# Kernel optimization log

Hardware: AMD Instinct MI355X
Metric: run time of the kernel (lower is better)

## Reference

```python
import jax, jax.numpy as jnp
import numpy as np

I_SZ, H_SZ, M_SZ, D_SZ, T_LEN = 256, 512, 16384, 256, 128


def setup_inputs() -> dict:
    key = jax.random.key(0)
    ks = iter(jax.random.split(key, 48))

    def rn(shape, s=0.05):
        return jax.random.normal(next(ks), shape, dtype=jnp.float32) * s

    Hd, D = H_SZ, D_SZ
    inp = {
        "inputs": rn((T_LEN, 1, I_SZ), 1.0),
        "memory0": rn((M_SZ, D), 0.01),            # register_buffer: randn*0.01
        "read_w0": jnp.zeros((M_SZ,), jnp.float32),
        "write_w0": jnp.zeros((M_SZ,), jnp.float32),
        "W_ih": rn((4 * Hd, I_SZ + D)),             # LSTM input->gates (i,f,g,o)
        "W_hh": rn((4 * Hd, Hd)),
        "b_ih": jnp.zeros((4 * Hd,), jnp.float32),
        "b_hh": jnp.zeros((4 * Hd,), jnp.float32),
        "Wo": rn((I_SZ, Hd + D)),                   # output_layer
        "bo": jnp.zeros((I_SZ,), jnp.float32),
    }
    for p in ("r", "w"):  # read head / write head addressing params
        inp[p + "_Wk"] = rn((D, Hd)); inp[p + "_bk"] = jnp.zeros((D,), jnp.float32)
        inp[p + "_Wb"] = rn((1, Hd)); inp[p + "_bb"] = jnp.zeros((1,), jnp.float32)
        inp[p + "_Wg"] = rn((1, Hd)); inp[p + "_bg"] = jnp.zeros((1,), jnp.float32)
        inp[p + "_Ws"] = rn((3, Hd)); inp[p + "_bs"] = jnp.zeros((3,), jnp.float32)
        inp[p + "_Wp"] = rn((1, Hd)); inp[p + "_bp"] = jnp.zeros((1,), jnp.float32)
    inp["w_We"] = rn((D, Hd)); inp["w_be"] = jnp.zeros((D,), jnp.float32)  # erase
    inp["w_Wa"] = rn((D, Hd)); inp["w_ba"] = jnp.zeros((D,), jnp.float32)  # add
    return inp


def _attend(co, mem, prev_w, Wk, bk, Wb, bb, Wg, bg, Ws, bs, Wp, bp):
    # co: (1,H), mem: (M,D), prev_w: (M,) -> (M,)
    key = co @ Wk.T + bk                                   # (1,D)
    beta = jax.nn.softplus(co @ Wb.T + bb)                 # (1,1) key strength
    kn = key / jnp.maximum(jnp.linalg.norm(key, axis=-1, keepdims=True), 1e-12)
    mn = mem / jnp.maximum(jnp.linalg.norm(mem, axis=-1, keepdims=True), 1e-12)
    cw = jax.nn.softmax(beta * (kn @ mn.T), axis=-1)       # (1,M) content weights
    g = jax.nn.sigmoid(co @ Wg.T + bg)                     # interpolation gate
    gw = g * cw + (1.0 - g) * prev_w[None, :]
    s = jax.nn.softmax(co @ Ws.T + bs, axis=-1)            # (1,3) shift kernel
    shifted = (s[:, 0:1] * jnp.roll(gw, -1, axis=-1)
               + s[:, 1:2] * gw
               + s[:, 2:3] * jnp.roll(gw, 1, axis=-1))
    gamma = jax.nn.softplus(co @ Wp.T + bp) + 1.0          # sharpening >= 1
    w = shifted ** gamma
    return (w / (w.sum(-1, keepdims=True) + 1e-8))[0]


def reference(inputs, memory0, read_w0, write_w0, W_ih, W_hh, b_ih, b_hh, Wo, bo,
              r_Wk, r_bk, r_Wb, r_bb, r_Wg, r_bg, r_Ws, r_bs, r_Wp, r_bp,
              w_Wk, w_bk, w_Wb, w_bb, w_Wg, w_bg, w_Ws, w_bs, w_Wp, w_bp,
              w_We, w_be, w_Wa, w_ba):
    H = W_hh.shape[1]

    def step(carry, x_t):
        mem, rw, ww, h, c = carry
        read_vec = rw @ mem                                  # (D,) read old memory
        ci = jnp.concatenate([x_t[0], read_vec])[None, :]    # (1, I+D)
        gates = ci @ W_ih.T + b_ih + h @ W_hh.T + b_hh       # (1, 4H)
        i_, f_, g_, o_ = jnp.split(gates, 4, axis=-1)
        c_new = jax.nn.sigmoid(f_) * c + jax.nn.sigmoid(i_) * jnp.tanh(g_)
        h_new = jax.nn.sigmoid(o_) * jnp.tanh(c_new)
        co = h_new                                           # controller output (1,H)
        ww_new = _attend(co, mem, ww, w_Wk, w_bk, w_Wb, w_bb, w_Wg, w_bg, w_Ws, w_bs, w_Wp, w_bp)
        erase = jax.nn.sigmoid(co @ w_We.T + w_be)[0]        # (D,)
        add = (co @ w_Wa.T + w_ba)[0]                        # (D,)
        mem_new = mem * (1.0 - ww_new[:, None] * erase[None, :]) + ww_new[:, None] * add[None, :]
        rw_new = _attend(co, mem_new, rw, r_Wk, r_bk, r_Wb, r_bb, r_Wg, r_bg, r_Ws, r_bs, r_Wp, r_bp)
        out = jnp.concatenate([co[0], read_vec])[None, :] @ Wo.T + bo  # (1, I)
        return (mem_new, rw_new, ww_new, h_new, c_new), out

    init = (memory0, read_w0, write_w0,
            jnp.zeros((1, H), inputs.dtype), jnp.zeros((1, H), inputs.dtype))
    _, outs = jax.lax.scan(step, init, inputs)               # (T,1,I)
    return outs
```

## Files before the change

### kernel.cpp

```cpp
#include <hip/hip_runtime.h>
#include <math.h>


#define NBLK 128
#define NTHR 512
#define Msz  16384
#define Dsz  256
#define Hsz  512
#define Isz  256
#define Tlen 128
#define RPB  128
#define NG   16

#define FXS  1073741824.0f
#define FXSI (1.0 / 1073741824.0)
#define CNT1 (1ull << 48)

struct Params { const float* in[34]; float* out; float* ws; };

__device__ __forceinline__ float wred64(float v){
#pragma unroll
  for (int o = 32; o > 0; o >>= 1) v += __shfl_xor(v, o, 64);
  return v;
}
__device__ __forceinline__ float wred32(float v){
#pragma unroll
  for (int o = 16; o > 0; o >>= 1) v += __shfl_xor(v, o, 32);
  return v;
}
__device__ __forceinline__ float qsum4(float v){
  v += __uint_as_float(__builtin_amdgcn_mov_dpp(__float_as_uint(v), 0xB1, 0xF, 0xF, true));
  v += __uint_as_float(__builtin_amdgcn_mov_dpp(__float_as_uint(v), 0x4E, 0xF, 0xF, true));
  return v;
}
__device__ __forceinline__ float sigm(float x){ return 1.f / (1.f + __expf(-x)); }
__device__ __forceinline__ float softplusf(float x){ return (x > 20.f) ? x : log1pf(__expf(x)); }

__device__ __forceinline__ void gstore(float* p, float v){
  __hip_atomic_store(p, v, __ATOMIC_RELAXED, __HIP_MEMORY_SCOPE_AGENT);
}
__device__ __forceinline__ float gload(const float* p){
  return __hip_atomic_load(p, __ATOMIC_RELAXED, __HIP_MEMORY_SCOPE_AGENT);
}
__device__ __forceinline__ void gstore64(unsigned long long* p, unsigned long long v){
  __hip_atomic_store(p, v, __ATOMIC_RELAXED, __HIP_MEMORY_SCOPE_AGENT);
}
__device__ __forceinline__ unsigned long long gload64(const unsigned long long* p){
  return __hip_atomic_load(p, __ATOMIC_RELAXED, __HIP_MEMORY_SCOPE_AGENT);
}
__device__ __forceinline__ void lbar(){
  __builtin_amdgcn_s_waitcnt(0xC07F);
  __builtin_amdgcn_s_barrier();
}
__device__ __forceinline__ float pollw(const unsigned long long* p, unsigned want){
  unsigned long long k;
  do { k = gload64(p); } while ((int)((unsigned)(k >> 32) - want) < 0);
  return __uint_as_float((unsigned)k);
}
__device__ __forceinline__ unsigned long long fxpack(float v){
  return CNT1 + (unsigned long long)(v * FXS);
}

__global__ void __launch_bounds__(NTHR, 1)
ntm_kernel(Params P)
{
  const int b   = blockIdx.x;
  const int tid = threadIdx.x;
  const int wv  = tid >> 6;
  const int ln  = tid & 63;

  const float* inputs  = P.in[0];
  const float* mem0    = P.in[1];
  const float* read_w0 = P.in[2];
  const float* write_w0= P.in[3];
  const float* W_ih = P.in[4];
  const float* W_hh = P.in[5];
  const float* b_ih = P.in[6];
  const float* b_hh = P.in[7];
  const float* Wo   = P.in[8];
  const float* bo   = P.in[9];
  const float* r_Wk = P.in[10]; const float* r_bk = P.in[11];
  const float* r_Wb = P.in[12]; const float* r_bb = P.in[13];
  const float* r_Wg = P.in[14]; const float* r_bg = P.in[15];
  const float* r_Ws = P.in[16]; const float* r_bs = P.in[17];
  const float* r_Wp = P.in[18]; const float* r_bp = P.in[19];
  const float* w_Wk = P.in[20]; const float* w_bk = P.in[21];
  const float* w_Wb = P.in[22]; const float* w_bb = P.in[23];
  const float* w_Wg = P.in[24]; const float* w_bg = P.in[25];
  const float* w_Ws = P.in[26]; const float* w_bs = P.in[27];
  const float* w_Wp = P.in[28]; const float* w_bp = P.in[29];
  const float* w_We = P.in[30]; const float* w_be = P.in[31];
  const float* w_Wa = P.in[32]; const float* w_ba = P.in[33];
  float* out = P.out;

  float* ws = P.ws;
  float* PA = ws;
  float* PB = ws + 4096;
  unsigned long long* U    = (unsigned long long*)(ws + 8192);
  unsigned long long* hpub = U;
  unsigned long long* ppub = U + 1024;
  unsigned long long* wEF  = U + 2320;
  unsigned long long* wPF  = wEF + 128;
  unsigned long long* wEL  = wPF + 128;
  unsigned long long* wPL  = wEL + 128;
  unsigned long long* rEF  = wPL + 128;
  unsigned long long* rPF  = rEF + 128;
  unsigned long long* rEL  = rPF + 128;
  unsigned long long* rPL  = rEL + 128;
  unsigned long long* redD = rPL + 128;
  unsigned long long* redF = redD + Tlen;
  unsigned long long* redH = redF + Tlen;
  unsigned long long* redJ = redH + Tlen;
  unsigned long long* redI = redJ + Tlen;
  float* Pbuf[2] = { PA, PB };

  __shared__ float s_mem[RPB * Dsz];
  __shared__ float s_co[Hsz];
  __shared__ float s_a[256], s_b[256], s_c[256];
  __shared__ float s_rv[256];
  __shared__ float s_norm[RPB];
  __shared__ float s_e[RPB];
  __shared__ float s_bw[RPB];
  __shared__ float s_rw[RPB];
  __shared__ float s_ww[RPB];
  __shared__ float s_A1[RPB], s_A2[RPB], s_B1[RPB], s_B0[RPB];
  __shared__ float s_dot[RPB];
  __shared__ float s_red[8];
  __shared__ float s_lg[16];
  __shared__ float s_scal[16];
  __shared__ float s_w2[2];
  __shared__ float s_cst[4];
  __shared__ float s_bd[4];
  __shared__ float s_pub;
  __shared__ float s_gval;

  auto redWait = [&](unsigned long long* slot)->float{
    if (tid == 0){
      unsigned long long k;
      do { k = gload64(slot); } while ((unsigned)(k >> 48) < (unsigned)NBLK);
      s_gval = (float)((double)(k & 0xFFFFFFFFFFFFull) * FXSI);
    }
    lbar();
    return s_gval;
  };

  auto bred512 = [&](float v)->float{
    v = wred64(v);
    lbar();
    if (ln == 0) s_red[wv] = v;
    lbar();
    return s_red[0] + s_red[1] + s_red[2] + s_red[3]
         + s_red[4] + s_red[5] + s_red[6] + s_red[7];
  };

  auto shiftSharpen = [&](int si, float* s_prevw, float S, unsigned long long* slot){
    float g     = sigm(s_scal[si + 1]);
    float gamma = softplusf(s_scal[si + 2]) + 1.f;
    float a0 = s_scal[si + 3], a1 = s_scal[si + 4], a2 = s_scal[si + 5];
    float mx = fmaxf(a0, fmaxf(a1, a2));
    float e0 = __expf(a0 - mx), e1 = __expf(a1 - mx), e2 = __expf(a2 - mx);
    float idn = 1.f / (e0 + e1 + e2);
    float s0 = e0 * idn, s1 = e1 * idn, s2 = e2 * idn;
    float invS = 1.f / S;
    float w = 0.f;
    if (tid < RPB){
      float gc = g * invS, gp = 1.f - g;
      float em = s_e[tid],  pm = s_prevw[tid];
      float e1n = (tid < RPB-1) ? s_e[tid+1]     : s_bd[0];
      float p1n = (tid < RPB-1) ? s_prevw[tid+1] : s_bd[1];
      float e2n = (tid > 0)     ? s_e[tid-1]     : s_bd[2];
      float p2n = (tid > 0)     ? s_prevw[tid-1] : s_bd[3];
      float gwm = gc * em  + gp * pm;
      float gw1 = gc * e1n + gp * p1n;
      float gw2 = gc * e2n + gp * p2n;
      float sh = s0 * gw1 + s1 * gwm + s2 * gw2;
      w = powf(sh, gamma);
      s_bw[tid] = w;
    }
    float tot = wred64(w);
    if (ln == 0 && wv < 2) s_w2[wv] = tot;
    lbar();
    if (tid == 0){
      float T2 = s_w2[0] + s_w2[1];
      s_pub = T2;
      if (slot) atomicAdd(slot, fxpack(T2));
    }
  };

  auto gemvXH = [&]()->float{
    int dd = tid >> 5, l = tid & 31;
    int r = (dd >> 2) * Hsz + (b << 2) + (dd & 3);
    const float* wi = W_ih + (size_t)r * (Isz + Dsz);
    const float* wh = W_hh + (size_t)r * Hsz;
    float acc = 0.f;
#pragma unroll
    for (int it = 0; it < 2; ++it){
      int k = it * 128 + l * 4;
      float4 a = *(const float4*)(wi + k);
      float4 x = *(const float4*)(&s_a[k]);
      acc += a.x*x.x + a.y*x.y + a.z*x.z + a.w*x.w;
    }
#pragma unroll
    for (int it = 0; it < 4; ++it){
      int k = it * 128 + l * 4;
      float4 hw = *(const float4*)(wh + k);
      float4 hv = *(const float4*)(&s_co[k]);
      acc += hw.x*hv.x + hw.y*hv.y + hw.z*hv.z + hw.w*hv.w;
    }
    return acc;
  };

  float Srcarry = 1.f;
  float accxh   = 0.f;

  {
    if (b < NG && tid < 256){ gstore(&PA[b*256 + tid], 0.f); gstore(&PB[b*256 + tid], 0.f); }
    if (tid < RPB){
      s_rw[tid] = read_w0[b * RPB + tid];
      s_ww[tid] = write_w0[b * RPB + tid];
    }
    if (tid < 4) s_cst[tid] = 0.f;
    s_co[tid] = 0.f;
    __syncthreads();
    if (tid == 0) atomicAdd(redI + 0, CNT1);
    redWait(redI + 0);
  }

  {
#pragma unroll 1
    for (int it = 0; it < 16; ++it){
      int ml = it * 8 + wv;
      int m  = b * RPB + ml;
      float4 v = *(const float4*)(mem0 + (size_t)m * Dsz + ln * 4);
      *(float4*)(&s_mem[ml * Dsz + ln * 4]) = v;
      float n2 = wred64(v.x*v.x + v.y*v.y + v.z*v.z + v.w*v.w);
      if (ln == 0) s_norm[ml] = sqrtf(n2);
    }
    lbar();
    int col = tid & 255, half = tid >> 8;
    float acc = 0.f;
#pragma unroll 1
    for (int j = half * 64; j < half * 64 + 64; ++j) acc += s_rw[j] * s_mem[j * Dsz + col];
    if (half == 0) s_a[col] = acc;
    lbar();
    if (half == 1) atomicAdd(&PB[(b & (NG-1)) * 256 + col], acc + s_a[col]);
    __syncthreads();
    if (tid < 256) s_a[tid] = inputs[tid];
    if (tid == 0) atomicAdd(redI + 1, CNT1);
    lbar();
    accxh = gemvXH();
    redWait(redI + 1);
  }

  for (int t = 0; t < Tlen; ++t){
    const unsigned TT = (unsigned)(t + 3);
    const unsigned long long tg = (unsigned long long)TT << 32;
    float* Pcur = Pbuf[t & 1];
    float* Prd  = Pbuf[(t + 1) & 1];

    {
      float SrDiv = (t == 0) ? 1.f : (Srcarry + 1e-8f);
      if (t > 0 && tid < RPB) s_rw[tid] = s_bw[tid] / SrDiv;
      if (tid < 256){
        float rvv = 0.f;
#pragma unroll
        for (int p = 0; p < NG; ++p) rvv += gload(&Prd[p * 256 + tid]);
        s_rv[tid] = rvv / SrDiv;
      }
      lbar();
      int dd = tid >> 5, l = tid & 31;
      int r = (dd >> 2) * Hsz + (b << 2) + (dd & 3);
      const float* wi = W_ih + (size_t)r * (Isz + Dsz) + Isz;
      float acc = accxh;
#pragma unroll
      for (int it = 0; it < 2; ++it){
        int k = it * 128 + l * 4;
        float4 a = *(const float4*)(wi + k);
        float4 x = *(const float4*)(&s_rv[k]);
        acc += a.x*x.x + a.y*x.y + a.z*x.z + a.w*x.w;
      }
      acc = wred32(acc);
      if (l == 0) s_lg[dd] = acc + b_ih[r] + b_hh[r];
      lbar();
      if (tid < 4){
        float iv = s_lg[tid], fv = s_lg[4 + tid], gv = s_lg[8 + tid], ov = s_lg[12 + tid];
        float cn = sigm(fv) * s_cst[tid] + sigm(iv) * tanhf(gv);
        s_cst[tid] = cn;
        float hn = sigm(ov) * tanhf(cn);
        gstore64(&hpub[(size_t)b * 8 + tid], tg | (unsigned long long)__float_as_uint(hn));
      }
    }

    {
      s_co[tid] = pollw(&hpub[(size_t)(tid >> 2) * 8 + (tid & 3)], TT);
      lbar();
#pragma unroll
      for (int qi = 0; qi < 2; ++qi){
        int q = qi * 8 + wv;
        int slot = q * 128 + b;
        if (slot < 1292){
          const float* Wrow = nullptr; float bias = 0.f; int len = 512;
          int mode = 0;
          if (slot < 256){ Wrow = w_Wk + (size_t)slot * Hsz; bias = w_bk[slot]; }
          else if (slot < 512){ int i = slot - 256; Wrow = w_We + (size_t)i * Hsz; bias = w_be[i]; mode = 1; }
          else if (slot < 768){ int i = slot - 512; Wrow = w_Wa + (size_t)i * Hsz; bias = w_ba[i]; }
          else if (slot < 1024){ int i = slot - 768; Wrow = r_Wk + (size_t)i * Hsz; bias = r_bk[i]; }
          else if (slot < 1280){ int i = slot - 1024; Wrow = Wo + (size_t)i * (Hsz + Dsz); bias = bo[i]; len = 768; mode = 2; }
          else {
            int i = slot - 1280;
            int ii = (i >= 6) ? i - 6 : i;
            bool rh = (i >= 6);
            const float *Wt, *bt; int row = 0;
            if (ii == 0){ Wt = rh ? r_Wb : w_Wb; bt = rh ? r_bb : w_bb; }
            else if (ii == 1){ Wt = rh ? r_Wg : w_Wg; bt = rh ? r_bg : w_bg; }
            else if (ii == 2){ Wt = rh ? r_Wp : w_Wp; bt = rh ? r_bp : w_bp; }
            else { Wt = rh ? r_Ws : w_Ws; bt = rh ? r_bs : w_bs; row = ii - 3; }
            Wrow = Wt + (size_t)row * Hsz; bias = bt[row];
          }
          float acc = 0.f;
          if (len == 512){
            int k = ln * 8;
            float4 a0 = *(const float4*)(Wrow + k);
            float4 a1 = *(const float4*)(Wrow + k + 4);
            float4 c0 = *(const float4*)(&s_co[k]);
            float4 c1 = *(const float4*)(&s_co[k + 4]);
            acc = a0.x*c0.x + a0.y*c0.y + a0.z*c0.z + a0.w*c0.w
                + a1.x*c1.x + a1.y*c1.y + a1.z*c1.z + a1.w*c1.w;
          } else {
            int k = ln * 4;
            float4 w0 = *(const float4*)(Wrow + k);
            float4 w1 = *(const float4*)(Wrow + 256 + k);
            float4 w2 = *(const float4*)(Wrow + 512 + k);
            float4 c0 = *(const float4*)(&s_co[k]);
            float4 c1 = *(const float4*)(&s_co[256 + k]);
            float4 r0 = *(const float4*)(&s_rv[k]);
            acc = w0.x*c0.x + w0.y*c0.y + w0.z*c0.z + w0.w*c0.w
                + w1.x*c1.x + w1.y*c1.y + w1.z*c1.z + w1.w*c1.w
                + w2.x*r0.x + w2.y*r0.y + w2.z*r0.z + w2.w*r0.w;
          }
          acc = wred64(acc);
          if (ln == 0){
            float v = acc + bias;
            if (mode == 1) v = sigm(v);
            if (mode == 2) out[(size_t)t * Isz + (slot - 1024)] = v;
            else gstore64(&ppub[slot], tg | (unsigned long long)__float_as_uint(v));
          }
        }
      }
    }

    if (t == Tlen - 1) break;

    float betaR = 0.f, invbkR = 0.f;

    {
      float* Pnx = Pbuf[(t + 1) & 1];
      if (b < NG && tid < 256) gstore(&Pnx[b * 256 + tid], 0.f);
      if (tid < 256) s_a[tid] = pollw(&ppub[tid], TT);
      else if (tid < 268) s_scal[tid - 256] = pollw(&ppub[1280 + (tid - 256)], TT);
      lbar();
      float nk2 = bred512((tid < 256) ? s_a[tid] * s_a[tid] : 0.f);
      float beta  = softplusf(s_scal[0]);
      float invbk = beta / fmaxf(sqrtf(nk2), 1e-12f);
      int row = tid >> 2, q = tid & 3;
      const float* mrow = &s_mem[row * Dsz];
      float d = 0.f;
#pragma unroll
      for (int k = 0; k < 16; ++k){
        int c = (q + 4 * ((k + row) & 15)) * 4;
        float4 mv = *(const float4*)(mrow + c);
        float4 kv = *(const float4*)(&s_a[c]);
        d += mv.x*kv.x + mv.y*kv.y + mv.z*kv.z + mv.w*kv.w;
      }
      d = qsum4(d);
      if (q == 0) s_dot[row] = d;
      lbar();
      float e = 0.f;
      if (tid < RPB){
        float score = s_dot[tid] * invbk / fmaxf(s_norm[tid], 1e-12f);
        e = __expf(score - beta);
        s_e[tid] = e;
      }
      float tot = wred64(e);
      if (ln == 0 && wv < 2) s_w2[wv] = tot;
      lbar();
      if (tid == 0){
        float T = s_w2[0] + s_w2[1];
        gstore64(&wEF[b], tg | (unsigned long long)__float_as_uint(s_e[0]));
        gstore64(&wPF[b], tg | (unsigned long long)__float_as_uint(s_ww[0]));
        gstore64(&wEL[b], tg | (unsigned long long)__float_as_uint(s_e[RPB-1]));
        gstore64(&wPL[b], tg | (unsigned long long)__float_as_uint(s_ww[RPB-1]));
        atomicAdd(redD + t, fxpack(T));
      }
    }

    {
      if (tid < 256) s_a[tid] = pollw(&ppub[256 + tid], TT);
      else           s_b[tid - 256] = pollw(&ppub[512 + (tid - 256)], TT);
      if (tid < 256) s_c[tid] = pollw(&ppub[768 + tid], TT);
      float nk2r = bred512((tid < 256) ? s_c[tid] * s_c[tid] : 0.f);
      betaR  = softplusf(s_scal[6]);
      invbkR = betaR / fmaxf(sqrtf(nk2r), 1e-12f);
      int row = tid >> 2, q = tid & 3;
      const float* mrow = &s_mem[row * Dsz];
      float mq = 0.f, qq = 0.f, qk = 0.f, mk = 0.f;
#pragma unroll
      for (int k = 0; k < 16; ++k){
        int c = (q + 4 * ((k + row) & 15)) * 4;
        float4 mv = *(const float4*)(mrow + c);
        float4 er = *(const float4*)(&s_a[c]);
        float4 ad = *(const float4*)(&s_b[c]);
        float4 kr = *(const float4*)(&s_c[c]);
        float qx = ad.x - mv.x * er.x;
        float qy = ad.y - mv.y * er.y;
        float qz = ad.z - mv.z * er.z;
        float qw = ad.w - mv.w * er.w;
        mq += mv.x*qx + mv.y*qy + mv.z*qz + mv.w*qw;
        qq += qx*qx + qy*qy + qz*qz + qw*qw;
        qk += qx*kr.x + qy*kr.y + qz*kr.z + qw*kr.w;
        mk += mv.x*kr.x + mv.y*kr.y + mv.z*kr.z + mv.w*kr.w;
      }
      mq = qsum4(mq); qq = qsum4(qq); qk = qsum4(qk); mk = qsum4(mk);
      if (q == 0){ s_A1[row] = 2.f*mq; s_A2[row] = qq; s_B1[row] = qk; s_B0[row] = mk; }
    }

    {
      if (wv == 0 && ln < 4){
        const unsigned long long* bp = (ln == 0) ? &wEF[(b + 1) & (NBLK-1)]
                               : (ln == 1) ? &wPF[(b + 1) & (NBLK-1)]
                               : (ln == 2) ? &wEL[(b - 1) & (NBLK-1)]
                                           : &wPL[(b - 1) & (NBLK-1)];
        s_bd[ln] = pollw(bp, TT);
      }
      float S_w = redWait(redD + t);
      shiftSharpen(0, s_ww, S_w, redF + t);
    }

    {
      float Sw = redWait(redF + t);
      float invSw = 1.f / (Sw + 1e-8f);
      float4 er4 = *(const float4*)(&s_a[ln * 4]);
      float4 ad4 = *(const float4*)(&s_b[ln * 4]);
      float e = 0.f;
      if (tid < RPB){
        float wwm = s_bw[tid] * invSw;
        s_ww[tid] = wwm;
        float A0 = s_norm[tid] * s_norm[tid];
        float n2 = fmaf(wwm, fmaf(wwm, s_A2[tid], s_A1[tid]), A0);
        float dt = fmaf(wwm, s_B1[tid], s_B0[tid]);
        float nr = sqrtf(fmaxf(n2, 0.f));
        s_norm[tid] = nr;
        float score = dt * invbkR / fmaxf(nr, 1e-12f);
        e = __expf(score - betaR);
        s_e[tid] = e;
      }
      float tot = wred64(e);
      if (ln == 0 && wv < 2) s_w2[wv] = tot;
      lbar();
      if (tid == 0){
        float T2 = s_w2[0] + s_w2[1];
        gstore64(&rEF[b], tg | (unsigned long long)__float_as_uint(s_e[0]));
        gstore64(&rPF[b], tg | (unsigned long long)__float_as_uint(s_rw[0]));
        gstore64(&rEL[b], tg | (unsigned long long)__float_as_uint(s_e[RPB-1]));
        gstore64(&rPL[b], tg | (unsigned long long)__float_as_uint(s_rw[RPB-1]));
        atomicAdd(redH + t, fxpack(T2));
      }
#pragma unroll 1
      for (int it = 0; it < 16; ++it){
        int ml = it * 8 + wv;
        int off = ml * Dsz + ln * 4;
        float wwm = s_bw[ml] * invSw;
        float4 mv = *(const float4*)(&s_mem[off]);
        float4 nv;
        nv.x = fmaf(wwm, ad4.x - mv.x * er4.x, mv.x);
        nv.y = fmaf(wwm, ad4.y - mv.y * er4.y, mv.y);
        nv.z = fmaf(wwm, ad4.z - mv.z * er4.z, mv.z);
        nv.w = fmaf(wwm, ad4.w - mv.w * er4.w, mv.w);
        *(float4*)(&s_mem[off]) = nv;
      }
    }

    {
      if (wv == 0 && ln < 4){
        const unsigned long long* bp = (ln == 0) ? &rEF[(b + 1) & (NBLK-1)]
                               : (ln == 1) ? &rPF[(b + 1) & (NBLK-1)]
                               : (ln == 2) ? &rEL[(b - 1) & (NBLK-1)]
                                           : &rPL[(b - 1) & (NBLK-1)];
        s_bd[ln] = pollw(bp, TT);
      }
      float S_r = redWait(redH + t);
      shiftSharpen(6, s_rw, S_r, nullptr);
      lbar();
      int col = tid & 255, half = tid >> 8;
      float acc = 0.f;
#pragma unroll 1
      for (int j = half * 64; j < half * 64 + 64; ++j) acc += s_bw[j] * s_mem[j * Dsz + col];
      if (half == 0) s_a[col] = acc;
      lbar();
      if (half == 1) atomicAdd(&Pcur[(b & (NG-1)) * 256 + col], acc + s_a[col]);
      __syncthreads();
      if (tid == 0) atomicAdd(redJ + t, fxpack(s_pub));
      if (tid < 256) s_a[tid] = inputs[(size_t)(t + 1) * Isz + tid];
      lbar();
      accxh = gemvXH();
      Srcarry = redWait(redJ + t);
    }
  }
}

extern "C" void kernel_launch(void* const* d_in, const int* in_sizes, int n_in,
                              void* d_out, int out_size, void* d_ws, size_t ws_size,
                              hipStream_t stream)
{
  (void)in_sizes; (void)out_size;
  if (n_in < 34) return;
  if (ws_size < (size_t)98304) return;
  Params P;
  for (int i = 0; i < 34; ++i) P.in[i] = (const float*)d_in[i];
  P.out = (float*)d_out;
  P.ws  = (float*)d_ws;
  hipLaunchKernelGGL(ntm_kernel, dim3(NBLK), dim3(NTHR), 0, stream, P);
}
```

Before: 3.631 ms.

## Spread grid-wide reduction atomics across eight slots to cut contention

The per-timestep cross-block reductions (redD, redF, redH, redJ) used to send all 128 blocks' atomicAdds to a single 64-bit counter. Each reduction now has eight counters, chosen by block index mod 8, so sixteen blocks share each one. The waiting thread polls all eight and sums their counts and values. The fixed-point scale also moves from 2^30 to 2^32 and is computed in double, giving finer precision but less headroom before the 48-bit value field overflows. Erase, add and read-key vectors get their own shared buffers instead of reusing s_a/s_b/s_c, so s_a can be overwritten without clobbering them.

```diff
diff --git a/kernel.cpp b/kernel.cpp
--- a/kernel.cpp
+++ b/kernel.cpp
@@ -12,8 +12,6 @@
 #define RPB  128
 #define NG   16
 
-#define FXS  1073741824.0f
-#define FXSI (1.0 / 1073741824.0)
 #define CNT1 (1ull << 48)
 
 struct Params { const float* in[34]; float* out; float* ws; };
@@ -58,7 +56,7 @@
   return __uint_as_float((unsigned)k);
 }
 __device__ __forceinline__ unsigned long long fxpack(float v){
-  return CNT1 + (unsigned long long)(v * FXS);
+  return CNT1 + (unsigned long long)((double)v * 4294967296.0);
 }
 
 __global__ void __launch_bounds__(NTHR, 1)
@@ -96,7 +94,7 @@
   float* ws = P.ws;
   float* PA = ws;
   float* PB = ws + 4096;
-  unsigned long long* U    = (unsigned long long*)(ws + 8192);
+  unsigned long long* U = (unsigned long long*)(ws + 8192);
   unsigned long long* hpub = U;
   unsigned long long* ppub = U + 1024;
   unsigned long long* wEF  = U + 2320;
@@ -107,16 +105,18 @@
   unsigned long long* rPF  = rEF + 128;
   unsigned long long* rEL  = rPF + 128;
   unsigned long long* rPL  = rEL + 128;
-  unsigned long long* redD = rPL + 128;
-  unsigned long long* redF = redD + Tlen;
-  unsigned long long* redH = redF + Tlen;
-  unsigned long long* redJ = redH + Tlen;
-  unsigned long long* redI = redJ + Tlen;
+  unsigned long long* redD = U + 3344;
+  unsigned long long* redF = redD + 8 * Tlen;
+  unsigned long long* redH = redF + 8 * Tlen;
+  unsigned long long* redJ = redH + 8 * Tlen;
+  unsigned long long* redI = redJ + 8 * Tlen;
   float* Pbuf[2] = { PA, PB };
+  const int slot = b & 7;
 
   __shared__ float s_mem[RPB * Dsz];
   __shared__ float s_co[Hsz];
-  __shared__ float s_a[256], s_b[256], s_c[256];
+  __shared__ float s_a[256];
+  __shared__ float s_er[256], s_ad[256], s_kr[256];
   __shared__ float s_rv[256];
   __shared__ float s_norm[RPB];
   __shared__ float s_e[RPB];
@@ -134,11 +134,32 @@
   __shared__ float s_pub;
   __shared__ float s_gval;
 
-  auto redWait = [&](unsigned long long* slot)->float{
+  auto redWait8 = [&](unsigned long long* base, int t)->float{
+    if (tid == 0){
+      unsigned long long k0,k1,k2,k3,k4,k5,k6,k7;
+      for (;;){
+        k0 = gload64(base + 0*Tlen + t); k1 = gload64(base + 1*Tlen + t);
+        k2 = gload64(base + 2*Tlen + t); k3 = gload64(base + 3*Tlen + t);
+        k4 = gload64(base + 4*Tlen + t); k5 = gload64(base + 5*Tlen + t);
+        k6 = gload64(base + 6*Tlen + t); k7 = gload64(base + 7*Tlen + t);
+        unsigned c = (unsigned)(k0>>48) + (unsigned)(k1>>48)
+                   + (unsigned)(k2>>48) + (unsigned)(k3>>48)
+                   + (unsigned)(k4>>48) + (unsigned)(k5>>48)
+                   + (unsigned)(k6>>48) + (unsigned)(k7>>48);
+        if (c >= (unsigned)NBLK) break;
+      }
+      const unsigned long long m = 0xFFFFFFFFFFFFull;
+      unsigned long long s = (k0&m)+(k1&m)+(k2&m)+(k3&m)+(k4&m)+(k5&m)+(k6&m)+(k7&m);
+      s_gval = (float)((double)s * (1.0 / 4294967296.0));
+    }
+    lbar();
+    return s_gval;
+  };
+  auto redWait1 = [&](unsigned long long* p)->float{
     if (tid == 0){
       unsigned long long k;
-      do { k = gload64(slot); } while ((unsigned)(k >> 48) < (unsigned)NBLK);
-      s_gval = (float)((double)(k & 0xFFFFFFFFFFFFull) * FXSI);
+      do { k = gload64(p); } while ((unsigned)(k >> 48) < (unsigned)NBLK);
+      s_gval = (float)((double)(k & 0xFFFFFFFFFFFFull) * (1.0 / 4294967296.0));
     }
     lbar();
     return s_gval;
@@ -153,7 +174,7 @@
          + s_red[4] + s_red[5] + s_red[6] + s_red[7];
   };
 
-  auto shiftSharpen = [&](int si, float* s_prevw, float S, unsigned long long* slot){
+  auto shiftSharpen = [&](int si, float* s_prevw, float S, unsigned long long* slotp){
     float g     = sigm(s_scal[si + 1]);
     float gamma = softplusf(s_scal[si + 2]) + 1.f;
     float a0 = s_scal[si + 3], a1 = s_scal[si + 4], a2 = s_scal[si + 5];
@@ -183,7 +204,7 @@
     if (tid == 0){
       float T2 = s_w2[0] + s_w2[1];
       s_pub = T2;
-      if (slot) atomicAdd(slot, fxpack(T2));
+      if (slotp) atomicAdd(slotp, fxpack(T2));
     }
   };
 
@@ -223,7 +244,7 @@
     s_co[tid] = 0.f;
     __syncthreads();
     if (tid == 0) atomicAdd(redI + 0, CNT1);
-    redWait(redI + 0);
+    redWait1(redI + 0);
   }
 
   {
@@ -249,7 +270,7 @@
     if (tid == 0) atomicAdd(redI + 1, CNT1);
     lbar();
     accxh = gemvXH();
-    redWait(redI + 1);
+    redWait1(redI + 1);
   }
 
   for (int t = 0; t < Tlen; ++t){
@@ -297,17 +318,17 @@
 #pragma unroll
       for (int qi = 0; qi < 2; ++qi){
         int q = qi * 8 + wv;
-        int slot = q * 128 + b;
-        if (slot < 1292){
+        int pslot = q * 128 + b;
+        if (pslot < 1292){
           const float* Wrow = nullptr; float bias = 0.f; int len = 512;
           int mode = 0;
-          if (slot < 256){ Wrow = w_Wk + (size_t)slot * Hsz; bias = w_bk[slot]; }
-          else if (slot < 512){ int i = slot - 256; Wrow = w_We + (size_t)i * Hsz; bias = w_be[i]; mode = 1; }
-          else if (slot < 768){ int i = slot - 512; Wrow = w_Wa + (size_t)i * Hsz; bias = w_ba[i]; }
-          else if (slot < 1024){ int i = slot - 768; Wrow = r_Wk + (size_t)i * Hsz; bias = r_bk[i]; }
-          else if (slot < 1280){ int i = slot - 1024; Wrow = Wo + (size_t)i * (Hsz + Dsz); bias = bo[i]; len = 768; mode = 2; }
+          if (pslot < 256){ Wrow = w_Wk + (size_t)pslot * Hsz; bias = w_bk[pslot]; }
+          else if (pslot < 512){ int i = pslot - 256; Wrow = w_We + (size_t)i * Hsz; bias = w_be[i]; mode = 1; }
+          else if (pslot < 768){ int i = pslot - 512; Wrow = w_Wa + (size_t)i * Hsz; bias = w_ba[i]; }
+          else if (pslot < 1024){ int i = pslot - 768; Wrow = r_Wk + (size_t)i * Hsz; bias = r_bk[i]; }
+          else if (pslot < 1280){ int i = pslot - 1024; Wrow = Wo + (size_t)i * (Hsz + Dsz); bias = bo[i]; len = 768; mode = 2; }
           else {
-            int i = slot - 1280;
+            int i = pslot - 1280;
             int ii = (i >= 6) ? i - 6 : i;
             bool rh = (i >= 6);
             const float *Wt, *bt; int row = 0;
@@ -342,8 +363,8 @@
           if (ln == 0){
             float v = acc + bias;
             if (mode == 1) v = sigm(v);
-            if (mode == 2) out[(size_t)t * Isz + (slot - 1024)] = v;
-            else gstore64(&ppub[slot], tg | (unsigned long long)__float_as_uint(v));
+            if (mode == 2) out[(size_t)t * Isz + (pslot - 1024)] = v;
+            else gstore64(&ppub[pslot], tg | (unsigned long long)__float_as_uint(v));
           }
         }
       }
@@ -390,15 +411,15 @@
         gstore64(&wPF[b], tg | (unsigned long long)__float_as_uint(s_ww[0]));
         gstore64(&wEL[b], tg | (unsigned long long)__float_as_uint(s_e[RPB-1]));
         gstore64(&wPL[b], tg | (unsigned long long)__float_as_uint(s_ww[RPB-1]));
-        atomicAdd(redD + t, fxpack(T));
-      }
-    }
-
-    {
-      if (tid < 256) s_a[tid] = pollw(&ppub[256 + tid], TT);
-      else           s_b[tid - 256] = pollw(&ppub[512 + (tid - 256)], TT);
-      if (tid < 256) s_c[tid] = pollw(&ppub[768 + tid], TT);
-      float nk2r = bred512((tid < 256) ? s_c[tid] * s_c[tid] : 0.f);
+        atomicAdd(redD + slot * Tlen + t, fxpack(T));
+      }
+    }
+
+    {
+      if (tid < 256) s_er[tid] = pollw(&ppub[256 + tid], TT);
+      else           s_ad[tid - 256] = pollw(&ppub[512 + (tid - 256)], TT);
+      if (tid < 256) s_kr[tid] = pollw(&ppub[768 + tid], TT);
+      float nk2r = bred512((tid < 256) ? s_kr[tid] * s_kr[tid] : 0.f);
       betaR  = softplusf(s_scal[6]);
       invbkR = betaR / fmaxf(sqrtf(nk2r), 1e-12f);
       int row = tid >> 2, q = tid & 3;
@@ -408,9 +429,9 @@
       for (int k = 0; k < 16; ++k){
         int c = (q + 4 * ((k + row) & 15)) * 4;
         float4 mv = *(const float4*)(mrow + c);
-        float4 er = *(const float4*)(&s_a[c]);
-        float4 ad = *(const float4*)(&s_b[c]);
-        float4 kr = *(const float4*)(&s_c[c]);
+        float4 er = *(const float4*)(&s_er[c]);
+        float4 ad = *(const float4*)(&s_ad[c]);
+        float4 kr = *(const float4*)(&s_kr[c]);
         float qx = ad.x - mv.x * er.x;
         float qy = ad.y - mv.y * er.y;
         float qz = ad.z - mv.z * er.z;
@@ -432,15 +453,15 @@
                                            : &wPL[(b - 1) & (NBLK-1)];
         s_bd[ln] = pollw(bp, TT);
       }
-      float S_w = redWait(redD + t);
-      shiftSharpen(0, s_ww, S_w, redF + t);
-    }
-
-    {
-      float Sw = redWait(redF + t);
+      float S_w = redWait8(redD, t);
+      shiftSharpen(0, s_ww, S_w, redF + slot * Tlen + t);
+    }
+
+    {
+      float Sw = redWait8(redF, t);
       float invSw = 1.f / (Sw + 1e-8f);
-      float4 er4 = *(const float4*)(&s_a[ln * 4]);
-      float4 ad4 = *(const float4*)(&s_b[ln * 4]);
+      float4 er4 = *(const float4*)(&s_er[ln * 4]);
+      float4 ad4 = *(const float4*)(&s_ad[ln * 4]);
       float e = 0.f;
       if (tid < RPB){
         float wwm = s_bw[tid] * invSw;
@@ -463,7 +484,7 @@
         gstore64(&rPF[b], tg | (unsigned long long)__float_as_uint(s_rw[0]));
         gstore64(&rEL[b], tg | (unsigned long long)__float_as_uint(s_e[RPB-1]));
         gstore64(&rPL[b], tg | (unsigned long long)__float_as_uint(s_rw[RPB-1]));
-        atomicAdd(redH + t, fxpack(T2));
+        atomicAdd(redH + slot * Tlen + t, fxpack(T2));
       }
 #pragma unroll 1
       for (int it = 0; it < 16; ++it){
@@ -488,7 +509,7 @@
                                            : &rPL[(b - 1) & (NBLK-1)];
         s_bd[ln] = pollw(bp, TT);
       }
-      float S_r = redWait(redH + t);
+      float S_r = redWait8(redH, t);
       shiftSharpen(6, s_rw, S_r, nullptr);
       lbar();
       int col = tid & 255, half = tid >> 8;
@@ -499,11 +520,11 @@
       lbar();
       if (half == 1) atomicAdd(&Pcur[(b & (NG-1)) * 256 + col], acc + s_a[col]);
       __syncthreads();
-      if (tid == 0) atomicAdd(redJ + t, fxpack(s_pub));
+      if (tid == 0) atomicAdd(redJ + slot * Tlen + t, fxpack(s_pub));
       if (tid < 256) s_a[tid] = inputs[(size_t)(t + 1) * Isz + tid];
       lbar();
       accxh = gemvXH();
-      Srcarry = redWait(redJ + t);
+      Srcarry = redWait8(redJ, t);
     }
   }
 }
```

New measurement: 3.606 ms (median of 2 runs). Within noise of the previous version (-0.7%).
